# Kernel tuning notes

Hardware: AMD Instinct MI355X
Metric: run time of the kernel (lower is better)

## Reference

```python
import jax, jax.numpy as jnp
import numpy as np


def _deconcat(values, offsets):
    """Ragged [N, D] + offsets [B+1] -> padded [B, L, D] and valid mask [B, L]."""
    offsets = np.asarray(offsets)
    lengths = np.diff(offsets)
    L = int(lengths.max())
    pos = np.arange(L)
    idx = np.minimum(offsets[:-1, None] + pos[None, :], values.shape[0] - 1)
    valid = pos[None, :] < lengths[:, None]  # [B, L]
    batched = jnp.take(values, jnp.asarray(idx), axis=0)
    batched = batched * jnp.asarray(valid, values.dtype)[:, :, None]
    return batched, jnp.asarray(valid)


def setup_inputs() -> dict:
    B, H, Wd, F, Q, D = 4, 128, 128, 16384, 300, 256
    key = jax.random.key(0)
    ks = jax.random.split(key, 8)
    queries = jax.random.normal(ks[0], (B * Q, D), jnp.float32)
    feature_values = jax.random.normal(ks[1], (B * F, D), jnp.float32)
    hw = jax.random.randint(ks[2], (B * F, 2), 0, H)
    bcol = jnp.repeat(jnp.arange(B), F)[:, None]
    feature_indices = jnp.concatenate([bcol, hw], axis=1).astype(jnp.int32)
    params = {}
    wkeys = jax.random.split(ks[3], 4)
    for i in range(4):
        params[f"W{i}"] = (jax.random.normal(wkeys[i], (D, D), jnp.float32) * 0.02)
        params[f"b{i}"] = jnp.zeros((D,), jnp.float32)
    return dict(
        queries=queries,
        feature_values=feature_values,
        feature_indices=feature_indices,
        query_batch_offsets=jnp.arange(B + 1, dtype=jnp.int32) * Q,
        feature_batch_offsets=jnp.arange(B + 1, dtype=jnp.int32) * F,
        height=H,
        width=Wd,
        **params,
    )


def reference(queries, feature_values, feature_indices,
              query_batch_offsets, feature_batch_offsets,
              height, width, W0, b0, W1, b1, W2, b2, W3, b3):
    q = queries
    for Wl, bl in ((W0, b0), (W1, b1), (W2, b2)):
        q = jax.nn.relu(q @ Wl.T + bl)
    q = q @ W3.T + b3

    bq, qvalid = _deconcat(q, query_batch_offsets)            # [B, Qm, D], [B, Qm]
    bf, fvalid = _deconcat(feature_values, feature_batch_offsets)  # [B, Fm, D]

    # bmm: per-image feature-vs-query logits
    logits = jnp.einsum('bfd,bqd->bfq', bf, bq)               # [B, Fm, Qm]

    # gather each real feature's logit row (undo padding), mask pad queries
    foff = jnp.asarray(np.asarray(feature_batch_offsets))
    b_of_n = feature_indices[:, 0]                            # [N]
    f_of_n = jnp.arange(feature_indices.shape[0]) - foff[b_of_n]
    flat = logits[b_of_n, f_of_n]                             # [N, Qm]
    flat = flat * qvalid.astype(logits.dtype)[b_of_n]

    # dense equivalent of the coalesced sparse COO output (B, H, W, Q);
    # duplicate (b,h,w) indices sum, matching coalesce()
    B, Qm = qvalid.shape
    out = jnp.zeros((B, height, width, Qm), logits.dtype)
    out = out.at[b_of_n, feature_indices[:, 1], feature_indices[:, 2]].add(flat)
    return out
```

## Files before the change

kernel.cpp:

```cpp
#include <hip/hip_runtime.h>
#include <hip/hip_bf16.h>
#include <stdint.h>

typedef __attribute__((ext_vector_type(8))) short bf16x8;
typedef __attribute__((ext_vector_type(4))) float f32x4;

__device__ __forceinline__ unsigned short f2bf(float f) {
    union { float f; unsigned u; } v; v.f = f;
    unsigned u = v.u;
    u += 0x7fff + ((u >> 16) & 1);
    return (unsigned short)(u >> 16);
}

__global__ __launch_bounds__(256) void prep(
    const int* __restrict__ FI, const int* __restrict__ wptr,
    int* __restrict__ cnt, int* __restrict__ slots,
    const float* __restrict__ W0, const float* __restrict__ W1,
    const float* __restrict__ W2, const float* __restrict__ W3,
    unsigned short* __restrict__ wsW,
    int NF, int HW, int wsz, int nbBin)
{
    int blk = blockIdx.x;
    if (blk < nbBin) {
        int i = blk * 256 + threadIdx.x;
        if (i >= NF) return;
        int Wd = *wptr;
        int b = FI[(size_t)i * 3];
        int h = FI[(size_t)i * 3 + 1];
        int w = FI[(size_t)i * 3 + 2];
        int gc = b * HW + h * Wd + w;
        int slot = atomicAdd(&cnt[gc], 1);
        if (slot < 16) slots[(size_t)gc * 16 + slot] = i;
    } else {
        int idx = ((blk - nbBin) * 256 + threadIdx.x) * 4;
        if (idx >= 4 * wsz) return;
        int l = idx / wsz, off = idx - l * wsz;
        const float* Ws = (l == 0) ? W0 : (l == 1) ? W1 : (l == 2) ? W2 : W3;
        float4 v = *(const float4*)(Ws + off);
        ushort4 o; o.x = f2bf(v.x); o.y = f2bf(v.y); o.z = f2bf(v.z); o.w = f2bf(v.w);
        *(ushort4*)(wsW + (size_t)l * wsz + off) = o;
    }
}

__global__ __launch_bounds__(256) void gather_mlp(
    const float* __restrict__ Qf, const unsigned short* __restrict__ Wb,
    const float* __restrict__ b0p, const float* __restrict__ b1p,
    const float* __restrict__ b2p, const float* __restrict__ b3p,
    unsigned short* __restrict__ outQB, int M, int wsz,
    const float* __restrict__ FV, const int* __restrict__ cnt,
    const int* __restrict__ slots, unsigned short* __restrict__ Abuf, int NC,
    int nbM, int nbG)
{
    __shared__ unsigned short At[16 * 264];
    const int tid = threadIdx.x;
    const int wid = tid >> 6, lane = tid & 63, quad = lane >> 4, l16 = lane & 15;

    if (blockIdx.x >= nbM) {
        const int hl  = lane & 31;
        const int hid = lane >> 5;
        const int wg = (blockIdx.x - nbM) * 4 + wid;
        const int nw = nbG * 4;
        for (int cb = wg * 4; cb < NC; cb += nw * 4) {
            int sl = slots[(size_t)cb * 16 + lane];
            #pragma unroll
            for (int i = 0; i < 2; ++i) {
                int j = i * 2 + hid;
                int c = cb + j;
                int nA = cnt[cb + i * 2];     if (nA > 16) nA = 16;
                int nB = cnt[cb + i * 2 + 1]; if (nB > 16) nB = 16;
                int n    = hid ? nB : nA;
                int nmax = nA > nB ? nA : nB;
                float4 a0 = make_float4(0.f, 0.f, 0.f, 0.f);
                float4 a1 = a0;
                for (int s = 0; s < nmax; ++s) {
                    int f = __shfl(sl, j * 16 + s);
                    if (s < n) {
                        const float* src = FV + (size_t)f * 256 + hl * 4;
                        float4 v0 = *(const float4*)(src);
                        float4 v1 = *(const float4*)(src + 128);
                        a0.x += v0.x; a0.y += v0.y; a0.z += v0.z; a0.w += v0.w;
                        a1.x += v1.x; a1.y += v1.y; a1.z += v1.z; a1.w += v1.w;
                    }
                }
                ushort4 o0, o1;
                o0.x = f2bf(a0.x); o0.y = f2bf(a0.y); o0.z = f2bf(a0.z); o0.w = f2bf(a0.w);
                o1.x = f2bf(a1.x); o1.y = f2bf(a1.y); o1.z = f2bf(a1.z); o1.w = f2bf(a1.w);
                unsigned short* dst = Abuf + (size_t)c * 256;
                *(ushort4*)(dst + hl * 4)       = o0;
                *(ushort4*)(dst + 128 + hl * 4) = o1;
            }
        }
        return;
    }

    const int m0 = blockIdx.x * 16;
    #pragma unroll
    for (int i = 0; i < 4; ++i) {
        int c = tid + i * 256;
        int row = c >> 6, kq = (c & 63) * 4;
        int gr = m0 + row; if (gr >= M) gr = M - 1;
        float4 v = *(const float4*)(Qf + (size_t)gr * 256 + kq);
        ushort4 o; o.x = f2bf(v.x); o.y = f2bf(v.y); o.z = f2bf(v.z); o.w = f2bf(v.w);
        *(ushort4*)&At[row * 264 + kq] = o;
    }
    __syncthreads();

    for (int l = 0; l < 4; ++l) {
        const unsigned short* Wl = Wb + (size_t)l * wsz;
        const float* bl = (l == 0) ? b0p : (l == 1) ? b1p : (l == 2) ? b2p : b3p;
        f32x4 acc[4] = {};
        #pragma unroll
        for (int k = 0; k < 256; k += 32) {
            bf16x8 af = *(const bf16x8*)&At[l16 * 264 + k + quad * 8];
            #pragma unroll
            for (int t = 0; t < 4; ++t) {
                int n = wid * 64 + t * 16 + l16;
                bf16x8 bfr = *(const bf16x8*)(Wl + (size_t)n * 256 + k + quad * 8);
                acc[t] = __builtin_amdgcn_mfma_f32_16x16x32_bf16(af, bfr, acc[t], 0, 0, 0);
            }
        }
        __syncthreads();
        #pragma unroll
        for (int t = 0; t < 4; ++t) {
            int n = wid * 64 + t * 16 + l16;
            float bv = bl[n];
            #pragma unroll
            for (int r = 0; r < 4; ++r) {
                int m = quad * 4 + r;
                float v = acc[t][r] + bv;
                if (l < 3) {
                    At[m * 264 + n] = f2bf(fmaxf(v, 0.f));
                } else {
                    if (m0 + m < M) outQB[(size_t)(m0 + m) * 256 + n] = f2bf(v);
                }
            }
        }
        if (l < 3) __syncthreads();
    }
}

__global__ __launch_bounds__(256, 4) void cell_gemm3(
    const unsigned short* __restrict__ Abuf,
    const unsigned short* __restrict__ QB, const int* __restrict__ qoff,
    float* __restrict__ out, int cpb, int HW, int Qstride)
{
    __shared__ unsigned short Bsm[304 * 40];

    const int tid = threadIdx.x;
    const int b   = blockIdx.x / cpb;
    const int c0  = (blockIdx.x - b * cpb) * 64;
    const size_t gc0 = (size_t)b * HW + c0;
    const int q0 = qoff[b];
    int qlen = qoff[b + 1] - q0; if (qlen < 1) qlen = 1;

    const int wid = tid >> 6, lane = tid & 63, quad = lane >> 4, l16 = lane & 15;

    const unsigned short* aptr = Abuf + (gc0 + wid * 16 + l16) * 256 + quad * 8;
    bf16x8 afA = *(const bf16x8*)aptr;
    f32x4 acc[19] = {};

    for (int k0 = 0; k0 < 256; k0 += 32) {
        for (int c = tid; c < 1216; c += 256) {
            int row = c >> 2, kc = (c & 3) * 8;
            int qr = row < qlen ? row : qlen - 1;
            uint4 v = *(const uint4*)(QB + (size_t)(q0 + qr) * 256 + k0 + kc);
            *(uint4*)&Bsm[row * 40 + kc] = v;
        }
        int k1 = (k0 + 32) & 255;
        bf16x8 afB = *(const bf16x8*)(aptr + k1);
        __syncthreads();
        #pragma unroll
        for (int t = 0; t < 19; ++t) {
            bf16x8 bfr = *(const bf16x8*)&Bsm[(t * 16 + l16) * 40 + quad * 8];
            acc[t] = __builtin_amdgcn_mfma_f32_16x16x32_bf16(afA, bfr, acc[t], 0, 0, 0);
        }
        __syncthreads();
        afA = afB;
    }

    #pragma unroll
    for (int r = 0; r < 4; ++r) {
        int m = quad * 4 + r;
        float* dst = out + (gc0 + wid * 16 + m) * Qstride;
        #pragma unroll
        for (int t = 0; t < 19; ++t) {
            int nq = t * 16 + l16;
            if (nq < Qstride) dst[nq] = (nq < qlen) ? acc[t][r] : 0.f;
        }
    }
}

extern "C" void kernel_launch(void* const* d_in, const int* in_sizes, int n_in,
                              void* d_out, int out_size, void* d_ws, size_t ws_size,
                              hipStream_t stream) {
    const float* queries = (const float*)d_in[0];
    const float* FV      = (const float*)d_in[1];
    const int*   FI      = (const int*)d_in[2];
    const int*   qoff    = (const int*)d_in[3];
    const int*   wptr    = (const int*)d_in[6];
    const float* W0 = (const float*)d_in[7];
    const float* b0 = (const float*)d_in[8];
    const float* W1 = (const float*)d_in[9];
    const float* b1 = (const float*)d_in[10];
    const float* W2 = (const float*)d_in[11];
    const float* b2 = (const float*)d_in[12];
    const float* W3 = (const float*)d_in[13];
    const float* b3 = (const float*)d_in[14];
    float* out = (float*)d_out;

    const int NQe = in_sizes[0];
    const int NQ  = NQe / 256;
    const int NF  = in_sizes[1] / 256;
    const int WSZ = in_sizes[7];
    const int B   = in_sizes[3] - 1;
    const int Q   = NQ / B;
    const int HW  = out_size / (B * Q);
    const int NC  = B * HW;
    const int cpb = HW / 64;

    int* cnt   = (int*)d_ws;
    int* slots = cnt + (size_t)NC;
    unsigned short* wsW  = (unsigned short*)(slots + (size_t)NC * 16);
    unsigned short* wsQB = wsW + (size_t)4 * WSZ;
    unsigned short* Abuf = wsQB + (size_t)NQe;

    hipMemsetAsync(cnt, 0, (size_t)NC * sizeof(int), stream);

    const int nbBin = (NF + 255) / 256;
    const int nbW   = (4 * WSZ / 4 + 255) / 256;
    prep<<<nbBin + nbW, 256, 0, stream>>>(FI, wptr, cnt, slots,
                                          W0, W1, W2, W3, wsW, NF, HW, WSZ, nbBin);

    const int nbM = (NQ + 15) / 16;
    const int nbG = 4096;
    gather_mlp<<<nbM + nbG, 256, 0, stream>>>(
        queries, wsW, b0, b1, b2, b3, wsQB, NQ, WSZ,
        FV, cnt, slots, Abuf, NC, nbM, nbG);

    cell_gemm3<<<B * cpb, 256, 0, stream>>>(Abuf, wsQB, qoff, out, cpb, HW, Q);
}
```

Baseline: 198.9 us.

## Double-buffer query tile via direct global-to-LDS loads with XOR swizzle

Replaces the register-staged copy of the query tile into shared memory with direct global-to-LDS loads into a double buffer, prefetching the next K-slice while the current one feeds the MFMAs. The padded LDS layout becomes a 32-wide layout with an XOR swizzle to avoid bank conflicts, and one barrier per iteration is dropped. The aim is to hide the global-load latency of the B operand. In exchange the kernel uses more LDS, which could lower occupancy, and it relies on the global_load_lds builtin being correct for this layout.

```diff
diff --git a/kernel.cpp b/kernel.cpp
--- a/kernel.cpp
+++ b/kernel.cpp
@@ -139,12 +139,12 @@
     }
 }
 
-__global__ __launch_bounds__(256, 4) void cell_gemm3(
+__global__ __launch_bounds__(256, 4) void cell_gemm10(
     const unsigned short* __restrict__ Abuf,
     const unsigned short* __restrict__ QB, const int* __restrict__ qoff,
     float* __restrict__ out, int cpb, int HW, int Qstride)
 {
-    __shared__ unsigned short Bsm[304 * 40];
+    __shared__ unsigned short Bsm[2][320 * 32];
 
     const int tid = threadIdx.x;
     const int b   = blockIdx.x / cpb;
@@ -155,28 +155,48 @@
 
     const int wid = tid >> 6, lane = tid & 63, quad = lane >> 4, l16 = lane & 15;
 
+    const unsigned short* gsrc[5];
+    #pragma unroll
+    for (int i = 0; i < 5; ++i) {
+        int c = tid + i * 256;
+        int row = c >> 2, sub = c & 3;
+        int qr = row < qlen ? row : qlen - 1;
+        gsrc[i] = QB + (size_t)(q0 + qr) * 256 + (sub ^ (row & 3)) * 8;
+    }
+
+    #define STAGE(s, kk)                                                      \
+        { _Pragma("unroll")                                                   \
+          for (int i = 0; i < 5; ++i)                                         \
+              __builtin_amdgcn_global_load_lds(                               \
+                  (const __attribute__((address_space(1))) unsigned int*)     \
+                      (gsrc[i] + (kk)),                                       \
+                  (__attribute__((address_space(3))) unsigned int*)           \
+                      &Bsm[s][(tid + i * 256) * 8],                           \
+                  16, 0, 0); }
+
     const unsigned short* aptr = Abuf + (gc0 + wid * 16 + l16) * 256 + quad * 8;
     bf16x8 afA = *(const bf16x8*)aptr;
     f32x4 acc[19] = {};
 
+    const int rslot = (quad ^ (l16 & 3)) * 8;
+
+    STAGE(0, 0);
+    __syncthreads();
+
     for (int k0 = 0; k0 < 256; k0 += 32) {
-        for (int c = tid; c < 1216; c += 256) {
-            int row = c >> 2, kc = (c & 3) * 8;
-            int qr = row < qlen ? row : qlen - 1;
-            uint4 v = *(const uint4*)(QB + (size_t)(q0 + qr) * 256 + k0 + kc);
-            *(uint4*)&Bsm[row * 40 + kc] = v;
-        }
+        const int cur = (k0 >> 5) & 1;
+        if (k0 + 32 < 256) STAGE(cur ^ 1, k0 + 32);
         int k1 = (k0 + 32) & 255;
         bf16x8 afB = *(const bf16x8*)(aptr + k1);
-        __syncthreads();
         #pragma unroll
         for (int t = 0; t < 19; ++t) {
-            bf16x8 bfr = *(const bf16x8*)&Bsm[(t * 16 + l16) * 40 + quad * 8];
+            bf16x8 bfr = *(const bf16x8*)&Bsm[cur][(t * 16 + l16) * 32 + rslot];
             acc[t] = __builtin_amdgcn_mfma_f32_16x16x32_bf16(afA, bfr, acc[t], 0, 0, 0);
         }
         __syncthreads();
         afA = afB;
     }
+    #undef STAGE
 
     #pragma unroll
     for (int r = 0; r < 4; ++r) {
@@ -237,5 +257,5 @@
         queries, wsW, b0, b1, b2, b3, wsQB, NQ, WSZ,
         FV, cnt, slots, Abuf, NC, nbM, nbG);
 
-    cell_gemm3<<<B * cpb, 256, 0, stream>>>(Abuf, wsQB, qoff, out, cpb, HW, Q);
-}
+    cell_gemm10<<<B * cpb, 256, 0, stream>>>(Abuf, wsQB, qoff, out, cpb, HW, Q);
+}
```

Result: faster. 194.6 us (-2.2%).
